# Kernel tuning notes

Measured on AMD Instinct MI355X. Metric: run time of the kernel, lower is better.

## Reference

```python
import jax, jax.numpy as jnp
import numpy as np

NUM_EXPERTS = 8
DIM = 2048
BATCH = 8192


def setup_inputs() -> dict:
    key = jax.random.key(0)
    k_x, k_ids, k_w, k_b = jax.random.split(key, 4)
    x = jax.random.normal(k_x, (BATCH, DIM), dtype=jnp.float32)
    cam_pred_ids = jax.random.randint(k_ids, (BATCH,), 0, NUM_EXPERTS, dtype=jnp.int64)
    # torch nn.Linear default init: U(-1/sqrt(in), 1/sqrt(in)); W is [out, in]
    bound = 1.0 / np.sqrt(DIM)
    W = jax.random.uniform(k_w, (NUM_EXPERTS, DIM, DIM), dtype=jnp.float32,
                           minval=-bound, maxval=bound)
    b = jax.random.uniform(k_b, (NUM_EXPERTS, DIM), dtype=jnp.float32,
                           minval=-bound, maxval=bound)
    return {"x": x, "cam_pred_ids": cam_pred_ids, "W": W, "b": b}


def reference(x, cam_pred_ids, W, b):
    # Per-sample expert routing: out[i] = x[i] + relu(x[i] @ W[e].T + b[e]),
    # where e = cam_pred_ids[i]. Vectorized as 8 full-batch GEMMs with masked
    # combine (fixed small expert count -> Python loop is structural, not data).
    h = jnp.zeros_like(x)
    for e in range(NUM_EXPERTS):
        he = jax.nn.relu(x @ W[e].T + b[e])          # [B, D]
        mask = (cam_pred_ids == e)[:, None]
        h = h + jnp.where(mask, he, jnp.zeros((), dtype=x.dtype))
    return x + h
```

## Files before the change

kernel.cpp:

```cpp
#include <hip/hip_runtime.h>
#include <hip/hip_bf16.h>
#include <stdint.h>

#define BATCH 8192
#define DIM   2048
#define NEXP  8
#define BM    128
#define BN    128
#define BK    64
#define MAX_TILES 72
#define NBLK  (DIM / BN)

typedef __bf16 bf16x8 __attribute__((ext_vector_type(8)));
typedef float  f32x4  __attribute__((ext_vector_type(4)));

#define XG_BYTE_OFF 40960ull
#define WB_BYTE_OFF 37789696ull
#define WS_NEED     104898560ull

#define AS1(p) ((const __attribute__((address_space(1))) void*)(p))
#define AS3(p) ((__attribute__((address_space(3))) void*)(p))

__device__ __forceinline__ unsigned f2bf2(float lo, float hi) {
    unsigned ul = __float_as_uint(lo), uh = __float_as_uint(hi);
    ul = (ul + 0x7FFFu + ((ul >> 16) & 1u)) >> 16;
    uh = (uh + 0x7FFFu + ((uh >> 16) & 1u)) >> 16;
    return (uh << 16) | ul;
}

__global__ void k_plan(const int* __restrict__ ids, int* __restrict__ ws) {
    __shared__ int sc[NEXP];
    int t = threadIdx.x;
    if (t < NEXP) sc[t] = 0;
    __syncthreads();
    for (int i = t; i < BATCH; i += 256) atomicAdd(&sc[ids[i]], 1);
    __syncthreads();
    if (t == 0) {
        int pos = 0, mt = 0;
        for (int e = 0; e < NEXP; e++) {
            int c = sc[e];
            ws[e]      = c;
            ws[16 + e] = 0;
            ws[32 + e] = pos;
            int ntl = (c + BM - 1) / BM;
            for (int tt = 0; tt < ntl; tt++) {
                ws[64  + mt] = e;
                ws[160 + mt] = pos + tt * BM;
                int v = c - tt * BM;
                ws[256 + mt] = v < BM ? v : BM;
                mt++;
            }
            pos += ntl * BM;
        }
        ws[48] = mt;
    }
}

__global__ void k_cvtW(const float4* __restrict__ W, uint2* __restrict__ Wb) {
    size_t i = (size_t)blockIdx.x * blockDim.x + threadIdx.x;
    float4 a = W[i];
    uint2 o;
    o.x = f2bf2(a.x, a.y);
    o.y = f2bf2(a.z, a.w);
    Wb[i] = o;
}

__global__ void k_gather(const float* __restrict__ x, const int* __restrict__ ids,
                         int* __restrict__ ws, unsigned short* __restrict__ xg,
                         int* __restrict__ rowmap) {
    int b = blockIdx.x;
    if (b >= BATCH) {
        int p = b - BATCH;
        int row = -1;
        for (int e = 0; e < NEXP; e++) {
            int c = ws[e];
            int pe = ((c + BM - 1) & ~(BM - 1)) - c;
            if (p < pe) { row = ws[32 + e] + c + p; break; }
            p -= pe;
        }
        if (row < 0) return;
        uint4* o = (uint4*)(xg + (size_t)row * DIM);
        uint4 z = make_uint4(0, 0, 0, 0);
        for (int t = threadIdx.x; t < DIM / 8; t += 256) o[t] = z;
        return;
    }
    __shared__ int spos;
    if (threadIdx.x == 0) {
        int e = ids[b];
        int p = ws[32 + e] + atomicAdd(&ws[16 + e], 1);
        spos = p;
        rowmap[p] = b;
    }
    __syncthreads();
    int pos = spos;
    const float4* xr = (const float4*)(x + (size_t)b * DIM);
    uint4* o = (uint4*)(xg + (size_t)pos * DIM);
    for (int t = threadIdx.x; t < DIM / 8; t += 256) {
        float4 a = xr[t * 2], b4 = xr[t * 2 + 1];
        uint4 v;
        v.x = f2bf2(a.x, a.y);  v.y = f2bf2(a.z, a.w);
        v.z = f2bf2(b4.x, b4.y); v.w = f2bf2(b4.z, b4.w);
        o[t] = v;
    }
}

__launch_bounds__(256)
__global__ void k_gemm(const unsigned short* __restrict__ xg,
                       const unsigned short* __restrict__ Wb,
                       const float* __restrict__ x, const float* __restrict__ bias,
                       const int* __restrict__ ws, const int* __restrict__ rowmap,
                       float* __restrict__ out) {
    int mt = blockIdx.y;
    if (mt >= ws[48]) return;
    int e     = ws[64  + mt];
    int pos0  = ws[160 + mt];
    int valid = ws[256 + mt];
    int n0 = blockIdx.x * BN;

    __shared__ unsigned short lA[BM * BK];
    __shared__ unsigned short lB[BN * BK];

    int tid = threadIdx.x;
    int w = tid >> 6, l = tid & 63;
    int lane15 = l & 15, quad = l >> 4;
    int wave_m = (w >> 1) * 64, wave_n = (w & 1) * 64;

    const unsigned short* Abase = xg + (size_t)pos0 * DIM;
    const unsigned short* Bbase = Wb + (size_t)e * DIM * DIM + (size_t)n0 * DIM;

    f32x4 acc[4][4];
#pragma unroll
    for (int i = 0; i < 4; i++)
#pragma unroll
        for (int j = 0; j < 4; j++) acc[i][j] = (f32x4){0.f, 0.f, 0.f, 0.f};

    int src_row[4], src_q[4];
#pragma unroll
    for (int j = 0; j < 4; j++) {
        int c = w * 256 + j * 64 + l;
        src_row[j] = c >> 3;
        src_q[j] = (c & 7) ^ (src_row[j] & 7);
    }

    for (int k0 = 0; k0 < DIM; k0 += BK) {
        __syncthreads();
#pragma unroll
        for (int j = 0; j < 4; j++) {
            __builtin_amdgcn_global_load_lds(
                AS1(Abase + (size_t)src_row[j] * DIM + k0 + src_q[j] * 8),
                AS3(lA + (w * 256 + j * 64) * 8), 16, 0, 0);
        }
#pragma unroll
        for (int j = 0; j < 4; j++) {
            __builtin_amdgcn_global_load_lds(
                AS1(Bbase + (size_t)src_row[j] * DIM + k0 + src_q[j] * 8),
                AS3(lB + (w * 256 + j * 64) * 8), 16, 0, 0);
        }
        __syncthreads();

#pragma unroll
        for (int s = 0; s < 2; s++) {
            bf16x8 af[4], bf[4];
            int q = s * 4 + quad;
#pragma unroll
            for (int mi = 0; mi < 4; mi++) {
                int r = wave_m + mi * 16 + lane15;
                af[mi] = *(const bf16x8*)(lA + r * BK + ((q ^ (r & 7)) * 8));
            }
#pragma unroll
            for (int ni = 0; ni < 4; ni++) {
                int r = wave_n + ni * 16 + lane15;
                bf[ni] = *(const bf16x8*)(lB + r * BK + ((q ^ (r & 7)) * 8));
            }
#pragma unroll
            for (int mi = 0; mi < 4; mi++)
#pragma unroll
                for (int ni = 0; ni < 4; ni++)
                    acc[mi][ni] = __builtin_amdgcn_mfma_f32_16x16x32_bf16(
                        af[mi], bf[ni], acc[mi][ni], 0, 0, 0);
        }
    }

    float bv[4];
#pragma unroll
    for (int ni = 0; ni < 4; ni++)
        bv[ni] = bias[(size_t)e * DIM + n0 + wave_n + ni * 16 + lane15];
#pragma unroll
    for (int mi = 0; mi < 4; mi++) {
#pragma unroll
        for (int r = 0; r < 4; r++) {
            int rl = wave_m + mi * 16 + quad * 4 + r;
            if (rl < valid) {
                int orig = rowmap[pos0 + rl];
                size_t rb = (size_t)orig * DIM;
#pragma unroll
                for (int ni = 0; ni < 4; ni++) {
                    int col = n0 + wave_n + ni * 16 + lane15;
                    float v = acc[mi][ni][r] + bv[ni];
                    v = v > 0.f ? v : 0.f;
                    out[rb + col] = x[rb + col] + v;
                }
            }
        }
    }
}

__global__ void k_naive(const float* __restrict__ x, const int* __restrict__ ids,
                        const float* __restrict__ W, const float* __restrict__ b,
                        float* __restrict__ out) {
    __shared__ float lx[DIM];
    int i = blockIdx.x;
    for (int t = threadIdx.x; t < DIM; t += blockDim.x) lx[t] = x[(size_t)i * DIM + t];
    __syncthreads();
    int e = ids[i];
    const float* We = W + (size_t)e * DIM * DIM;
    for (int n = threadIdx.x; n < DIM; n += blockDim.x) {
        const float* wr = We + (size_t)n * DIM;
        float acc = 0.f;
        for (int k = 0; k < DIM; k += 4) {
            float4 w4 = *(const float4*)(wr + k);
            acc += lx[k] * w4.x + lx[k + 1] * w4.y + lx[k + 2] * w4.z + lx[k + 3] * w4.w;
        }
        float v = acc + b[(size_t)e * DIM + n];
        v = v > 0.f ? v : 0.f;
        out[(size_t)i * DIM + n] = lx[n] + v;
    }
}

extern "C" void kernel_launch(void* const* d_in, const int* in_sizes, int n_in,
                              void* d_out, int out_size, void* d_ws, size_t ws_size,
                              hipStream_t stream) {
    const float* x   = (const float*)d_in[0];
    const int*   ids = (const int*)d_in[1];
    const float* W   = (const float*)d_in[2];
    const float* b   = (const float*)d_in[3];
    float* out = (float*)d_out;

    if (ws_size < WS_NEED) {
        k_naive<<<BATCH, 256, 0, stream>>>(x, ids, W, b, out);
        return;
    }

    char* wsb = (char*)d_ws;
    int*  wsi = (int*)wsb;
    unsigned short* xg = (unsigned short*)(wsb + XG_BYTE_OFF);
    unsigned short* Wb = (unsigned short*)(wsb + WB_BYTE_OFF);
    int* rowmap = wsi + 512;

    k_plan<<<1, 256, 0, stream>>>(ids, wsi);
    k_cvtW<<<(NEXP * DIM * DIM / 4) / 256, 256, 0, stream>>>((const float4*)W, (uint2*)Wb);
    k_gather<<<BATCH + 1024, 256, 0, stream>>>(x, ids, wsi, xg, rowmap);

    dim3 g(NBLK, MAX_TILES);
    k_gemm<<<g, 256, 0, stream>>>(xg, Wb, x, b, wsi, rowmap, out);
}
```

Measured before the change: 462.4 us.

## Double-buffer GEMM LDS tiles with BK=32 and read residual from bf16 xg

Restructures the GEMM main loop into a double-buffered pipeline with half-size K tiles. The next tile's global-to-LDS load is issued right after a single barrier, while MFMAs run on the current buffer, so load latency is meant to overlap compute. The epilogue now takes the residual x from the gathered bf16 copy, read contiguously by sorted position, instead of the scattered fp32 input. That lowers epilogue memory traffic but puts bf16 rounding error into the residual term.

After: 461.0 us. Within noise of the previous version (-0.3%).

```diff
diff --git a/kernel.cpp b/kernel.cpp
--- a/kernel.cpp
+++ b/kernel.cpp
@@ -7,7 +7,8 @@
 #define NEXP  8
 #define BM    128
 #define BN    128
-#define BK    64
+#define BK    32
+#define NITER (DIM / BK)
 #define MAX_TILES 72
 #define NBLK  (DIM / BN)
 
@@ -107,7 +108,7 @@
 __launch_bounds__(256)
 __global__ void k_gemm(const unsigned short* __restrict__ xg,
                        const unsigned short* __restrict__ Wb,
-                       const float* __restrict__ x, const float* __restrict__ bias,
+                       const float* __restrict__ bias,
                        const int* __restrict__ ws, const int* __restrict__ rowmap,
                        float* __restrict__ out) {
     int mt = blockIdx.y;
@@ -117,8 +118,7 @@
     int valid = ws[256 + mt];
     int n0 = blockIdx.x * BN;
 
-    __shared__ unsigned short lA[BM * BK];
-    __shared__ unsigned short lB[BN * BK];
+    __shared__ unsigned short lds[2][8192];
 
     int tid = threadIdx.x;
     int w = tid >> 6, l = tid & 63;
@@ -128,58 +128,67 @@
     const unsigned short* Abase = xg + (size_t)pos0 * DIM;
     const unsigned short* Bbase = Wb + (size_t)e * DIM * DIM + (size_t)n0 * DIM;
 
+    int srcOff[2];
+#pragma unroll
+    for (int j = 0; j < 2; j++) {
+        int c = w * 128 + j * 64 + l;
+        int row = c >> 2, pos = c & 3;
+        int q = pos ^ ((row >> 1) & 3);
+        srcOff[j] = row * DIM + q * 8;
+    }
+
+    int swz = (quad ^ ((lane15 >> 1) & 3)) * 8;
+    int afOff[4], bfOff[4];
+#pragma unroll
+    for (int mi = 0; mi < 4; mi++)
+        afOff[mi] = (wave_m + mi * 16 + lane15) * BK + swz;
+#pragma unroll
+    for (int ni = 0; ni < 4; ni++)
+        bfOff[ni] = 4096 + (wave_n + ni * 16 + lane15) * BK + swz;
+
     f32x4 acc[4][4];
 #pragma unroll
     for (int i = 0; i < 4; i++)
 #pragma unroll
         for (int j = 0; j < 4; j++) acc[i][j] = (f32x4){0.f, 0.f, 0.f, 0.f};
 
-    int src_row[4], src_q[4];
-#pragma unroll
-    for (int j = 0; j < 4; j++) {
-        int c = w * 256 + j * 64 + l;
-        src_row[j] = c >> 3;
-        src_q[j] = (c & 7) ^ (src_row[j] & 7);
-    }
-
-    for (int k0 = 0; k0 < DIM; k0 += BK) {
+#define ISSUE(buf, k0)                                                          \
+    do {                                                                        \
+        _Pragma("unroll")                                                       \
+        for (int j = 0; j < 2; j++) {                                           \
+            __builtin_amdgcn_global_load_lds(                                   \
+                AS1(Abase + (k0) + srcOff[j]),                                  \
+                AS3(&lds[buf][w * 1024 + j * 512]), 16, 0, 0);                  \
+            __builtin_amdgcn_global_load_lds(                                   \
+                AS1(Bbase + (k0) + srcOff[j]),                                  \
+                AS3(&lds[buf][4096 + w * 1024 + j * 512]), 16, 0, 0);           \
+        }                                                                       \
+    } while (0)
+
+    ISSUE(0, 0);
+    int cur = 0;
+    for (int i = 0; i < NITER; ++i) {
         __syncthreads();
-#pragma unroll
-        for (int j = 0; j < 4; j++) {
-            __builtin_amdgcn_global_load_lds(
-                AS1(Abase + (size_t)src_row[j] * DIM + k0 + src_q[j] * 8),
-                AS3(lA + (w * 256 + j * 64) * 8), 16, 0, 0);
-        }
-#pragma unroll
-        for (int j = 0; j < 4; j++) {
-            __builtin_amdgcn_global_load_lds(
-                AS1(Bbase + (size_t)src_row[j] * DIM + k0 + src_q[j] * 8),
-                AS3(lB + (w * 256 + j * 64) * 8), 16, 0, 0);
-        }
-        __syncthreads();
-
-#pragma unroll
-        for (int s = 0; s < 2; s++) {
-            bf16x8 af[4], bf[4];
-            int q = s * 4 + quad;
-#pragma unroll
-            for (int mi = 0; mi < 4; mi++) {
-                int r = wave_m + mi * 16 + lane15;
-                af[mi] = *(const bf16x8*)(lA + r * BK + ((q ^ (r & 7)) * 8));
-            }
-#pragma unroll
-            for (int ni = 0; ni < 4; ni++) {
-                int r = wave_n + ni * 16 + lane15;
-                bf[ni] = *(const bf16x8*)(lB + r * BK + ((q ^ (r & 7)) * 8));
-            }
-#pragma unroll
-            for (int mi = 0; mi < 4; mi++)
-#pragma unroll
-                for (int ni = 0; ni < 4; ni++)
-                    acc[mi][ni] = __builtin_amdgcn_mfma_f32_16x16x32_bf16(
-                        af[mi], bf[ni], acc[mi][ni], 0, 0, 0);
-        }
-    }
+        if (i + 1 < NITER) {
+            int k0n = (i + 1) * BK;
+            ISSUE(cur ^ 1, k0n);
+        }
+        bf16x8 af[4], bf[4];
+#pragma unroll
+        for (int mi = 0; mi < 4; mi++)
+            af[mi] = *(const bf16x8*)(&lds[cur][afOff[mi]]);
+#pragma unroll
+        for (int ni = 0; ni < 4; ni++)
+            bf[ni] = *(const bf16x8*)(&lds[cur][bfOff[ni]]);
+#pragma unroll
+        for (int mi = 0; mi < 4; mi++)
+#pragma unroll
+            for (int ni = 0; ni < 4; ni++)
+                acc[mi][ni] = __builtin_amdgcn_mfma_f32_16x16x32_bf16(
+                    af[mi], bf[ni], acc[mi][ni], 0, 0, 0);
+        cur ^= 1;
+    }
+#undef ISSUE
 
     float bv[4];
 #pragma unroll
@@ -192,13 +201,15 @@
             int rl = wave_m + mi * 16 + quad * 4 + r;
             if (rl < valid) {
                 int orig = rowmap[pos0 + rl];
-                size_t rb = (size_t)orig * DIM;
+                const unsigned short* xrow = xg + (size_t)(pos0 + rl) * DIM + n0;
+                float* orow = out + (size_t)orig * DIM + n0;
 #pragma unroll
                 for (int ni = 0; ni < 4; ni++) {
-                    int col = n0 + wave_n + ni * 16 + lane15;
+                    int col = wave_n + ni * 16 + lane15;
+                    float xv = __uint_as_float((unsigned)xrow[col] << 16);
                     float v = acc[mi][ni][r] + bv[ni];
                     v = v > 0.f ? v : 0.f;
-                    out[rb + col] = x[rb + col] + v;
+                    orow[col] = xv + v;
                 }
             }
         }
@@ -252,5 +263,5 @@
     k_gather<<<BATCH + 1024, 256, 0, stream>>>(x, ids, wsi, xg, rowmap);
 
     dim3 g(NBLK, MAX_TILES);
-    k_gemm<<<g, 256, 0, stream>>>(xg, Wb, x, b, wsi, rowmap, out);
-}
+    k_gemm<<<g, 256, 0, stream>>>(xg, Wb, b, wsi, rowmap, out);
+}
```
